# Kernel tuning notes

Measured on AMD Instinct MI355X. Metric: run time of the kernel, lower is better.

## Reference

```python
import jax, jax.numpy as jnp
import numpy as np

D = 1024      # total input features
R = 32        # number of ragged regions
RMAX = 32     # max region size (padding target)
HIDDEN = [128, 128]
H1, H2 = HIDDEN
B = 8192      # batch size


def _made_masks(r, rmax, hidden):
    """TFP AutoregressiveNetwork masks (left-to-right order, 'equal' hidden degrees,
    params=2, use_bias=False), zero-padded to rmax features."""
    order = np.arange(1, r + 1)
    degs = [order]
    for u in hidden:
        mn = min(int(degs[-1].min()), r - 1)
        degs.append(np.maximum(mn, np.ceil(np.arange(1, u + 1) * (r - 1) / float(u + 1)).astype(np.int64)))
    m1 = np.zeros((rmax, hidden[0]), bool)
    m1[:r] = degs[0][:, None] <= degs[1][None, :]
    m2 = degs[1][:, None] <= degs[2][None, :]
    mout = np.zeros((hidden[-1], rmax * 2), bool)
    out_deg = np.repeat(order, 2)  # output layout is feature-major: [feat, param]
    mout[:, :2 * r] = degs[-1][:, None] < out_deg[None, :]
    return m1, m2, mout


def setup_inputs() -> dict:
    rng = np.random.default_rng(0)
    perm = rng.permutation(D)
    sizes = rng.integers(8, RMAX + 1, size=R)
    idx = np.zeros((R, RMAX), np.int64)
    valid = np.zeros((R, RMAX), bool)
    M1 = np.zeros((R, RMAX, H1), bool)
    M2 = np.zeros((R, H1, H2), bool)
    Mout = np.zeros((R, H2, RMAX * 2), bool)
    pos = 0
    for i in range(R):
        s = int(sizes[i])
        idx[i, :s] = perm[pos:pos + s]
        pos += s
        valid[i, :s] = True
        M1[i], M2[i], Mout[i] = _made_masks(s, RMAX, HIDDEN)
    key = jax.random.key(0)
    k1, k2, k3, k4 = jax.random.split(key, 4)
    inputs = jax.random.normal(k1, (B, D), jnp.float32)
    W1 = jax.random.normal(k2, (R, RMAX, H1), jnp.float32) / np.float32(np.sqrt(RMAX))
    W2 = jax.random.normal(k3, (R, H1, H2), jnp.float32) / np.float32(np.sqrt(H1))
    Wout = jax.random.normal(k4, (R, H2, RMAX * 2), jnp.float32) / np.float32(np.sqrt(H2))
    return {"inputs": inputs, "W1": W1, "W2": W2, "Wout": Wout,
            "idx": jnp.asarray(idx), "valid": jnp.asarray(valid),
            "M1": jnp.asarray(M1), "M2": jnp.asarray(M2), "Mout": jnp.asarray(Mout)}


def reference(inputs, W1, W2, Wout, idx, valid, M1, M2, Mout):
    f = inputs.dtype
    v = valid.astype(f)                              # [R, RMAX]
    xg = jnp.take(inputs, idx, axis=1) * v           # [B, R, RMAX] ragged gather (padded)
    # MADE masked MLP (relu, no bias), batched over all regions at once
    h1 = jax.nn.relu(jnp.einsum('brd,rdh->brh', xg, W1 * M1.astype(f)))
    h2 = jax.nn.relu(jnp.einsum('brh,rhk->brk', h1, W2 * M2.astype(f)))
    out = jnp.einsum('brk,rko->bro', h2, Wout * Mout.astype(f))
    out = out.reshape(out.shape[0], out.shape[1], RMAX, 2)
    shift, log_s = out[..., 0], out[..., 1]
    # MAF inverse: u = (x - shift) * exp(-log_scale); logdet = -sum(log_scale)
    u = (xg - shift) * jnp.exp(-log_s)
    elem = -0.5 * u * u - 0.5 * jnp.log(2.0 * jnp.pi) - log_s
    ll = jnp.sum(elem * v, axis=-1)                  # [B, R]
    return ll[..., None]                             # [B, R, 1] as in tf.stack of expand_dims
```

## Files before the change

### kernel.cpp

```cpp
#include <hip/hip_runtime.h>
#include <math.h>


#define RR 32
#define DD 1024
#define HH 128
#define OO 64
#define TROWS 32
#define TILES 16
#define BLOCKS_PER_R 16

#define SHP 136
#define SXG 40
#define SSC 136

typedef _Float16 f16x8_t __attribute__((ext_vector_type(8)));
typedef float f32x4_t __attribute__((ext_vector_type(4)));
typedef unsigned short u16;
typedef unsigned int u32;

__device__ __forceinline__ u16 f16b(float x) {
    _Float16 h = (_Float16)x;
    union { _Float16 f; u16 u; } c; c.f = h; return c.u;
}
__device__ __forceinline__ f32x4_t mfma16h(f16x8_t a, f16x8_t b, f32x4_t c) {
    return __builtin_amdgcn_mfma_f32_16x16x32_f16(a, b, c, 0, 0, 0);
}

__device__ __forceinline__ void stage_block16(const float* __restrict__ W,
                                              const int* __restrict__ M,
                                              int ldc, int c0, int K, u16* dst,
                                              int tid)
{
    const int kb = tid >> 3;
    const int cb = tid & 7;
    if (kb * 4 >= K) return;
    const int k0 = kb * 4;
    float e[4][4];
#pragma unroll
    for (int i = 0; i < 4; ++i) {
        const int o = ((k0 + i) * ldc + c0 + 4 * cb) >> 2;
        float4 w = ((const float4*)W)[o];
        int4   m = ((const int4*)M)[o];
        e[i][0] = m.x ? w.x : 0.f; e[i][1] = m.y ? w.y : 0.f;
        e[i][2] = m.z ? w.z : 0.f; e[i][3] = m.w ? w.w : 0.f;
    }
#pragma unroll
    for (int j = 0; j < 4; ++j) {
        ushort4 p;
        p.x = f16b(e[0][j]); p.y = f16b(e[1][j]);
        p.z = f16b(e[2][j]); p.w = f16b(e[3][j]);
        *(ushort4*)&dst[(4 * cb + j) * SSC + k0] = p;
    }
}

__device__ __forceinline__ void relu_store16(u16* __restrict__ dst, int o, f32x4_t a)
{
    ushort4 s;
    s.x = f16b(fmaxf(a[0], 0.f));
    s.y = f16b(fmaxf(a[1], 0.f));
    s.z = f16b(fmaxf(a[2], 0.f));
    s.w = f16b(fmaxf(a[3], 0.f));
    *(ushort4*)&dst[o] = s;
}

__global__ __launch_bounds__(512, 6)
void made_flow_r21(const float* __restrict__ inputs,
                   const float* __restrict__ W1,
                   const float* __restrict__ W2,
                   const float* __restrict__ Wout,
                   const int* __restrict__ idx,
                   const int* __restrict__ valid,
                   const int* __restrict__ M1,
                   const int* __restrict__ M2,
                   const int* __restrict__ Mout,
                   float* __restrict__ out)
{
    __shared__ __align__(16) u16 h1s[TROWS * SHP];
    __shared__ __align__(16) u16 h2s[TROWS * SHP];
    __shared__ __align__(16) u16 wout_lds[OO * SSC];
    __shared__ __align__(16) u16 xgh[2][TROWS * SXG];
    __shared__ __align__(16) float red2[2][TROWS][4];
    __shared__ int   idx_s[RR];
    __shared__ float v_s[RR];

    u16* const scr  = h1s;
    u16* const scr2 = h2s;

    const int tid  = threadIdx.x;
    const int r    = blockIdx.x / BLOCKS_PER_R;
    const int rb   = blockIdx.x % BLOCKS_PER_R;
    const int ts   = rb * TILES;

    const int lane = tid & 63;
    const int wave = tid >> 6;
    const int q    = lane >> 4;
    const int l16  = lane & 15;
    const int wm3  = wave & 3;
    const int ni3  = wave >> 2;

    if (tid < RR) {
        idx_s[tid] = idx[r * RR + tid];
        v_s[tid]   = valid[r * RR + tid] ? 1.f : 0.f;
    }

    f16x8_t a1;
    f16x8_t a2[4];
    {
        const float* W1r = W1 + r * RR * HH;   const int* M1r = M1 + r * RR * HH;
        const float* W2r = W2 + r * HH * HH;   const int* M2r = M2 + r * HH * HH;
        const float* Wor = Wout + r * HH * OO; const int* Mor = Mout + r * HH * OO;
        const int c = wave >> 1, h = wave & 1;
        for (int i = 0; i < 2; ++i) {
            __syncthreads();
            if (tid < 256) stage_block16(W2r, M2r, HH, 32 * (2 * i),     HH, scr,  tid);
            else           stage_block16(W2r, M2r, HH, 32 * (2 * i + 1), HH, scr2, tid - 256);
            __syncthreads();
            if (c == 2 * i) {
#pragma unroll
                for (int ks = 0; ks < 4; ++ks)
                    a2[ks] = *(const f16x8_t*)&scr[(16 * h + l16) * SSC + ks * 32 + q * 8];
            } else if (c == 2 * i + 1) {
#pragma unroll
                for (int ks = 0; ks < 4; ++ks)
                    a2[ks] = *(const f16x8_t*)&scr2[(16 * h + l16) * SSC + ks * 32 + q * 8];
            }
        }
        for (int i = 0; i < 2; ++i) {
            __syncthreads();
            if (tid < 256) stage_block16(W1r, M1r, HH, 32 * (2 * i),     RR, scr,  tid);
            else           stage_block16(W1r, M1r, HH, 32 * (2 * i + 1), RR, scr2, tid - 256);
            __syncthreads();
            if (c == 2 * i)          a1 = *(const f16x8_t*)&scr [(16 * h + l16) * SSC + q * 8];
            else if (c == 2 * i + 1) a1 = *(const f16x8_t*)&scr2[(16 * h + l16) * SSC + q * 8];
        }
        if (tid < 256) stage_block16(Wor, Mor, OO, 0,  HH, wout_lds,            tid);
        else           stage_block16(Wor, Mor, OO, 32, HH, wout_lds + 32 * SSC, tid - 256);
    }
    __syncthreads();

    const f32x4_t zero4 = {0.f, 0.f, 0.f, 0.f};
    const int grow = tid >> 4;
    const int gg   = tid & 15;
    const int   ci0 = idx_s[2 * gg], ci1 = idx_s[2 * gg + 1];
    const float cv0 = v_s[2 * gg],   cv1 = v_s[2 * gg + 1];
    const int j0  = 8 * wm3 + 2 * q;
    const float vj0 = v_s[j0], vj1 = v_s[j0 + 1];
    const int gbase = (ts * TROWS + grow) * DD;

    float gx0, gx1;
    {
        float a0  = inputs[gbase + ci0] * cv0;
        float a1v = inputs[gbase + ci1] * cv1;
        *(u32*)&xgh[0][grow * SXG + 2 * gg] = (u32)f16b(a0) | ((u32)f16b(a1v) << 16);
        gx0 = inputs[gbase + TROWS * DD + ci0] * cv0;
        gx1 = inputs[gbase + TROWS * DD + ci1] * cv1;
    }
    __syncthreads();

    {
#pragma unroll
        for (int ni = 0; ni < 2; ++ni) {
            f16x8_t b = *(const f16x8_t*)&xgh[0][(16 * ni + l16) * SXG + q * 8];
            f32x4_t a = mfma16h(a1, b, zero4);
            relu_store16(h1s, (16 * ni + l16) * SHP + 16 * wave + 4 * q, a);
        }
    }

    for (int t = 0; t < TILES; ++t) {
        __syncthreads();

        const bool dg = (t + 1 < TILES);

        if (dg) {
            *(u32*)&xgh[(t + 1) & 1][grow * SXG + 2 * gg] =
                (u32)f16b(gx0) | ((u32)f16b(gx1) << 16);
        }
        {
            f32x4_t acc[2] = {zero4, zero4};
#pragma unroll
            for (int ks = 0; ks < 4; ++ks) {
#pragma unroll
                for (int ni = 0; ni < 2; ++ni) {
                    f16x8_t b = *(const f16x8_t*)&h1s[(16 * ni + l16) * SHP + ks * 32 + q * 8];
                    acc[ni] = mfma16h(a2[ks], b, acc[ni]);
                }
            }
#pragma unroll
            for (int ni = 0; ni < 2; ++ni)
                relu_store16(h2s, (16 * ni + l16) * SHP + 16 * wave + 4 * q, acc[ni]);
        }
        if (t >= 2 && tid < TROWS) {
            float4 rv = *(const float4*)&red2[t & 1][tid][0];
            out[((ts + (t - 2)) * TROWS + tid) * RR + r] =
                rv.x + rv.y + rv.z + rv.w;
        }
        __syncthreads();

        if (t + 2 < TILES) {
            const int base = gbase + (t + 2) * (TROWS * DD);
            gx0 = inputs[base + ci0] * cv0;
            gx1 = inputs[base + ci1] * cv1;
        }

        f32x4_t acc3 = zero4;
#pragma unroll
        for (int ks = 0; ks < 4; ++ks) {
            f16x8_t ao = *(const f16x8_t*)&wout_lds[(16 * wm3 + l16) * SSC + ks * 32 + q * 8];
            f16x8_t b  = *(const f16x8_t*)&h2s[(16 * ni3 + l16) * SHP + ks * 32 + q * 8];
            acc3 = mfma16h(ao, b, acc3);
        }

        if (dg) {
#pragma unroll
            for (int ni = 0; ni < 2; ++ni) {
                f16x8_t b = *(const f16x8_t*)&xgh[(t + 1) & 1][(16 * ni + l16) * SXG + q * 8];
                f32x4_t a = mfma16h(a1, b, zero4);
                relu_store16(h1s, (16 * ni + l16) * SHP + 16 * wave + 4 * q, a);
            }
        }

        {
            const int row = 16 * ni3 + l16;
            u32 xw = *(const u32*)&xgh[t & 1][row * SXG + j0];
            union { u32 u; _Float16 h[2]; } xc; xc.u = xw;
            const float xv0 = (float)xc.h[0], xv1 = (float)xc.h[1];
            const float u0 = (xv0 - acc3[0]) * __expf(-acc3[1]);
            const float u1 = (xv1 - acc3[2]) * __expf(-acc3[3]);
            float p = (-0.5f * u0 * u0 - 0.91893853320467266954f - acc3[1]) * vj0
                    + (-0.5f * u1 * u1 - 0.91893853320467266954f - acc3[3]) * vj1;
            p += __shfl_xor(p, 16, 64);
            p += __shfl_xor(p, 32, 64);
            if (q == 0) red2[t & 1][row][wm3] = p;
        }
    }

    __syncthreads();
    if (tid < 2 * TROWS) {
        const int tt  = TILES - 2 + (tid >> 5);
        const int row = tid & 31;
        float4 rv = *(const float4*)&red2[tt & 1][row][0];
        out[((ts + tt) * TROWS + row) * RR + r] =
            rv.x + rv.y + rv.z + rv.w;
    }
}

extern "C" void kernel_launch(void* const* d_in, const int* in_sizes, int n_in,
                              void* d_out, int out_size, void* d_ws, size_t ws_size,
                              hipStream_t stream)
{
    const float* inputs = (const float*)d_in[0];
    const float* W1     = (const float*)d_in[1];
    const float* W2     = (const float*)d_in[2];
    const float* Wout   = (const float*)d_in[3];
    const int*   idx    = (const int*)d_in[4];
    const int*   valid  = (const int*)d_in[5];
    const int*   M1     = (const int*)d_in[6];
    const int*   M2     = (const int*)d_in[7];
    const int*   Mout   = (const int*)d_in[8];
    float*       out    = (float*)d_out;

    hipLaunchKernelGGL(made_flow_r21, dim3(RR * BLOCKS_PER_R), dim3(512), 0, stream,
                       inputs, W1, W2, Wout, idx, valid, M1, M2, Mout, out);
}
```

Baseline: 123.3 us.

## Double row tile to 64 rows per step and use packed f16 conversion

Each block now processes 64 batch rows per tile over 8 tiles instead of 32 rows over 16 tiles. This halves the number of barrier-separated pipeline steps and lets each wave issue more independent MFMAs per step with reused weight fragments. Scalar f16 conversions are replaced with the packed round-toward-zero cvt_pkrtz intrinsic. LDS buffers and register use grow, and launch bounds drop to 4 blocks per CU. RTZ rounding slightly changes numerics.

Measured after the change: 121.1 us. No clear change (-1.7%).

```diff
diff --git a/kernel.cpp b/kernel.cpp
--- a/kernel.cpp
+++ b/kernel.cpp
@@ -6,8 +6,8 @@
 #define DD 1024
 #define HH 128
 #define OO 64
-#define TROWS 32
-#define TILES 16
+#define TROWS 64
+#define TILES 8
 #define BLOCKS_PER_R 16
 
 #define SHP 136
@@ -19,9 +19,10 @@
 typedef unsigned short u16;
 typedef unsigned int u32;
 
-__device__ __forceinline__ u16 f16b(float x) {
-    _Float16 h = (_Float16)x;
-    union { _Float16 f; u16 u; } c; c.f = h; return c.u;
+__device__ __forceinline__ u32 pkrtz(float a, float b) {
+    union { __fp16 v __attribute__((ext_vector_type(2))); u32 u; } c;
+    c.v = __builtin_amdgcn_cvt_pkrtz(a, b);
+    return c.u;
 }
 __device__ __forceinline__ f32x4_t mfma16h(f16x8_t a, f16x8_t b, f32x4_t c) {
     return __builtin_amdgcn_mfma_f32_16x16x32_f16(a, b, c, 0, 0, 0);
@@ -47,25 +48,23 @@
     }
 #pragma unroll
     for (int j = 0; j < 4; ++j) {
-        ushort4 p;
-        p.x = f16b(e[0][j]); p.y = f16b(e[1][j]);
-        p.z = f16b(e[2][j]); p.w = f16b(e[3][j]);
-        *(ushort4*)&dst[(4 * cb + j) * SSC + k0] = p;
+        uint2 p;
+        p.x = pkrtz(e[0][j], e[1][j]);
+        p.y = pkrtz(e[2][j], e[3][j]);
+        *(uint2*)&dst[(4 * cb + j) * SSC + k0] = p;
     }
 }
 
 __device__ __forceinline__ void relu_store16(u16* __restrict__ dst, int o, f32x4_t a)
 {
-    ushort4 s;
-    s.x = f16b(fmaxf(a[0], 0.f));
-    s.y = f16b(fmaxf(a[1], 0.f));
-    s.z = f16b(fmaxf(a[2], 0.f));
-    s.w = f16b(fmaxf(a[3], 0.f));
-    *(ushort4*)&dst[o] = s;
-}
-
-__global__ __launch_bounds__(512, 6)
-void made_flow_r21(const float* __restrict__ inputs,
+    uint2 s;
+    s.x = pkrtz(fmaxf(a[0], 0.f), fmaxf(a[1], 0.f));
+    s.y = pkrtz(fmaxf(a[2], 0.f), fmaxf(a[3], 0.f));
+    *(uint2*)&dst[o] = s;
+}
+
+__global__ __launch_bounds__(512, 4)
+void made_flow_r23(const float* __restrict__ inputs,
                    const float* __restrict__ W1,
                    const float* __restrict__ W2,
                    const float* __restrict__ Wout,
@@ -90,7 +89,7 @@
     const int tid  = threadIdx.x;
     const int r    = blockIdx.x / BLOCKS_PER_R;
     const int rb   = blockIdx.x % BLOCKS_PER_R;
-    const int ts   = rb * TILES;
+    const int ts64 = rb * TILES * TROWS;
 
     const int lane = tid & 63;
     const int wave = tid >> 6;
@@ -146,21 +145,25 @@
     const float cv0 = v_s[2 * gg],   cv1 = v_s[2 * gg + 1];
     const int j0  = 8 * wm3 + 2 * q;
     const float vj0 = v_s[j0], vj1 = v_s[j0 + 1];
-    const int gbase = (ts * TROWS + grow) * DD;
-
-    float gx0, gx1;
+    const int gb0 = (ts64 + grow) * DD;
+    const int gb1 = (ts64 + 32 + grow) * DD;
+
+    float gx[4];
     {
-        float a0  = inputs[gbase + ci0] * cv0;
-        float a1v = inputs[gbase + ci1] * cv1;
-        *(u32*)&xgh[0][grow * SXG + 2 * gg] = (u32)f16b(a0) | ((u32)f16b(a1v) << 16);
-        gx0 = inputs[gbase + TROWS * DD + ci0] * cv0;
-        gx1 = inputs[gbase + TROWS * DD + ci1] * cv1;
+        float a0 = inputs[gb0 + ci0] * cv0, a1v = inputs[gb0 + ci1] * cv1;
+        float b0 = inputs[gb1 + ci0] * cv0, b1v = inputs[gb1 + ci1] * cv1;
+        *(u32*)&xgh[0][grow * SXG + 2 * gg]        = pkrtz(a0, a1v);
+        *(u32*)&xgh[0][(grow + 32) * SXG + 2 * gg] = pkrtz(b0, b1v);
+        gx[0] = inputs[gb0 + TROWS * DD + ci0] * cv0;
+        gx[1] = inputs[gb0 + TROWS * DD + ci1] * cv1;
+        gx[2] = inputs[gb1 + TROWS * DD + ci0] * cv0;
+        gx[3] = inputs[gb1 + TROWS * DD + ci1] * cv1;
     }
     __syncthreads();
 
     {
 #pragma unroll
-        for (int ni = 0; ni < 2; ++ni) {
+        for (int ni = 0; ni < 4; ++ni) {
             f16x8_t b = *(const f16x8_t*)&xgh[0][(16 * ni + l16) * SXG + q * 8];
             f32x4_t a = mfma16h(a1, b, zero4);
             relu_store16(h1s, (16 * ni + l16) * SHP + 16 * wave + 4 * q, a);
@@ -173,62 +176,69 @@
         const bool dg = (t + 1 < TILES);
 
         if (dg) {
-            *(u32*)&xgh[(t + 1) & 1][grow * SXG + 2 * gg] =
-                (u32)f16b(gx0) | ((u32)f16b(gx1) << 16);
+            *(u32*)&xgh[(t + 1) & 1][grow * SXG + 2 * gg]        = pkrtz(gx[0], gx[1]);
+            *(u32*)&xgh[(t + 1) & 1][(grow + 32) * SXG + 2 * gg] = pkrtz(gx[2], gx[3]);
         }
         {
-            f32x4_t acc[2] = {zero4, zero4};
+            f32x4_t acc[4] = {zero4, zero4, zero4, zero4};
 #pragma unroll
             for (int ks = 0; ks < 4; ++ks) {
 #pragma unroll
-                for (int ni = 0; ni < 2; ++ni) {
+                for (int ni = 0; ni < 4; ++ni) {
                     f16x8_t b = *(const f16x8_t*)&h1s[(16 * ni + l16) * SHP + ks * 32 + q * 8];
                     acc[ni] = mfma16h(a2[ks], b, acc[ni]);
                 }
             }
 #pragma unroll
-            for (int ni = 0; ni < 2; ++ni)
+            for (int ni = 0; ni < 4; ++ni)
                 relu_store16(h2s, (16 * ni + l16) * SHP + 16 * wave + 4 * q, acc[ni]);
         }
         if (t >= 2 && tid < TROWS) {
             float4 rv = *(const float4*)&red2[t & 1][tid][0];
-            out[((ts + (t - 2)) * TROWS + tid) * RR + r] =
+            out[((rb * TILES + (t - 2)) * TROWS + tid) * RR + r] =
                 rv.x + rv.y + rv.z + rv.w;
         }
         __syncthreads();
 
         if (t + 2 < TILES) {
-            const int base = gbase + (t + 2) * (TROWS * DD);
-            gx0 = inputs[base + ci0] * cv0;
-            gx1 = inputs[base + ci1] * cv1;
-        }
-
-        f32x4_t acc3 = zero4;
+            const int base = (t + 2) * (TROWS * DD);
+            gx[0] = inputs[gb0 + base + ci0] * cv0;
+            gx[1] = inputs[gb0 + base + ci1] * cv1;
+            gx[2] = inputs[gb1 + base + ci0] * cv0;
+            gx[3] = inputs[gb1 + base + ci1] * cv1;
+        }
+
+        f32x4_t acc3[2] = {zero4, zero4};
 #pragma unroll
         for (int ks = 0; ks < 4; ++ks) {
             f16x8_t ao = *(const f16x8_t*)&wout_lds[(16 * wm3 + l16) * SSC + ks * 32 + q * 8];
-            f16x8_t b  = *(const f16x8_t*)&h2s[(16 * ni3 + l16) * SHP + ks * 32 + q * 8];
-            acc3 = mfma16h(ao, b, acc3);
+#pragma unroll
+            for (int nn = 0; nn < 2; ++nn) {
+                f16x8_t b = *(const f16x8_t*)&h2s[(16 * (ni3 + 2 * nn) + l16) * SHP + ks * 32 + q * 8];
+                acc3[nn] = mfma16h(ao, b, acc3[nn]);
+            }
         }
 
         if (dg) {
 #pragma unroll
-            for (int ni = 0; ni < 2; ++ni) {
+            for (int ni = 0; ni < 4; ++ni) {
                 f16x8_t b = *(const f16x8_t*)&xgh[(t + 1) & 1][(16 * ni + l16) * SXG + q * 8];
                 f32x4_t a = mfma16h(a1, b, zero4);
                 relu_store16(h1s, (16 * ni + l16) * SHP + 16 * wave + 4 * q, a);
             }
         }
 
-        {
-            const int row = 16 * ni3 + l16;
+#pragma unroll
+        for (int nn = 0; nn < 2; ++nn) {
+            const int row = 16 * (ni3 + 2 * nn) + l16;
             u32 xw = *(const u32*)&xgh[t & 1][row * SXG + j0];
             union { u32 u; _Float16 h[2]; } xc; xc.u = xw;
             const float xv0 = (float)xc.h[0], xv1 = (float)xc.h[1];
-            const float u0 = (xv0 - acc3[0]) * __expf(-acc3[1]);
-            const float u1 = (xv1 - acc3[2]) * __expf(-acc3[3]);
-            float p = (-0.5f * u0 * u0 - 0.91893853320467266954f - acc3[1]) * vj0
-                    + (-0.5f * u1 * u1 - 0.91893853320467266954f - acc3[3]) * vj1;
+            f32x4_t a = acc3[nn];
+            const float u0 = (xv0 - a[0]) * __expf(-a[1]);
+            const float u1 = (xv1 - a[2]) * __expf(-a[3]);
+            float p = (-0.5f * u0 * u0 - 0.91893853320467266954f - a[1]) * vj0
+                    + (-0.5f * u1 * u1 - 0.91893853320467266954f - a[3]) * vj1;
             p += __shfl_xor(p, 16, 64);
             p += __shfl_xor(p, 32, 64);
             if (q == 0) red2[t & 1][row][wm3] = p;
@@ -237,10 +247,10 @@
 
     __syncthreads();
     if (tid < 2 * TROWS) {
-        const int tt  = TILES - 2 + (tid >> 5);
-        const int row = tid & 31;
+        const int tt  = TILES - 2 + (tid >> 6);
+        const int row = tid & 63;
         float4 rv = *(const float4*)&red2[tt & 1][row][0];
-        out[((ts + tt) * TROWS + row) * RR + r] =
+        out[((rb * TILES + tt) * TROWS + row) * RR + r] =
             rv.x + rv.y + rv.z + rv.w;
     }
 }
@@ -260,6 +270,6 @@
     const int*   Mout   = (const int*)d_in[8];
     float*       out    = (float*)d_out;
 
-    hipLaunchKernelGGL(made_flow_r21, dim3(RR * BLOCKS_PER_R), dim3(512), 0, stream,
+    hipLaunchKernelGGL(made_flow_r23, dim3(RR * BLOCKS_PER_R), dim3(512), 0, stream,
                        inputs, W1, W2, Wout, idx, valid, M1, M2, Mout, out);
 }
```
